# Kernel optimization log

Measured on AMD Instinct MI355X. Metric: run time of the kernel, lower is better.

The kernel has to match this reference:

```python
import jax, jax.numpy as jnp
import numpy as np
from functools import partial

DIM = 192
HEADS = 8
DN = ('NCHW', 'OIHW', 'NCHW')


def conv1x1(x, w):
    # w: [O, I, 1, 1]
    return jax.lax.conv_general_dilated(x, w, (1, 1), 'VALID', dimension_numbers=DN)


def dwconv3x3(x, w):
    # w: [C, 1, 3, 3], depthwise
    return jax.lax.conv_general_dilated(x, w, (1, 1), 'SAME', dimension_numbers=DN,
                                        feature_group_count=x.shape[1])


def l2norm(x, eps=1e-12):
    n = jnp.sqrt(jnp.sum(x * x, axis=-1, keepdims=True))
    return x / jnp.maximum(n, eps)


def compute_attention(q, k_s, v_s, k_c, v_c, temperature, beta):
    b, c, h, w = q.shape
    hw = h * w
    r = lambda t: t.reshape(b, HEADS, c // HEADS, hw)  # b head c (h w)
    qn = l2norm(r(q))
    ks = l2norm(r(k_s))
    kc = l2norm(r(k_c))
    vs, vc = r(v_s), r(v_c)
    # channel-wise attention: [b, head, c, c]
    sa = jax.nn.softmax(jnp.einsum('bhcn,bhdn->bhcd', qn, ks) * temperature, axis=-1)
    so = jnp.einsum('bhcd,bhdn->bhcn', sa, vs)
    ca = jax.nn.softmax(-(jnp.einsum('bhcn,bhdn->bhcd', qn, kc) * temperature), axis=-1)
    co = jnp.einsum('bhcd,bhdn->bhcn', ca, vc)
    out = jax.nn.sigmoid(beta) * so + co
    return out.reshape(b, c, h, w)


def setup_inputs() -> dict:
    key = jax.random.key(0)
    ks = jax.random.split(key, 8)
    B, C, H, W = 8, DIM, 128, 128
    s = 0.02
    return {
        'x1': jax.random.normal(ks[0], (B, C, H, W), jnp.float32),
        'x2': jax.random.normal(ks[1], (B, C, H, W), jnp.float32),
        'w_qkv1': jax.random.normal(ks[2], (3 * C, C, 1, 1), jnp.float32) * s,
        'w_dw1': jax.random.normal(ks[3], (3 * C, 1, 3, 3), jnp.float32) * s,
        'w_qkv2': jax.random.normal(ks[4], (3 * C, C, 1, 1), jnp.float32) * s,
        'w_dw2': jax.random.normal(ks[5], (3 * C, 1, 3, 3), jnp.float32) * s,
        'w_proj': jax.random.normal(ks[6], (C, C, 1, 1), jnp.float32) * s,
        'temperature': jnp.ones((HEADS, 1, 1), jnp.float32),
        'beta': jnp.zeros((1,), jnp.float32),
    }


def reference(x1, x2, w_qkv1, w_dw1, w_qkv2, w_dw2, w_proj, temperature, beta):
    qkv1 = dwconv3x3(conv1x1(x1, w_qkv1), w_dw1)
    q1, k1, v1 = jnp.split(qkv1, 3, axis=1)
    qkv2 = dwconv3x3(conv1x1(x2, w_qkv2), w_dw2)
    q2, k2, v2 = jnp.split(qkv2, 3, axis=1)
    e1 = compute_attention(q1, k1, v1, k2, v2, temperature, beta)
    e2 = compute_attention(q2, k2, v2, k1, v1, temperature, beta)
    return conv1x1(e1, w_proj), conv1x1(e2, w_proj)
```

## Files before the change

kernel.cpp:

```cpp
#include <hip/hip_runtime.h>

typedef unsigned short u16;
typedef unsigned int u32;

#define NB 8
#define NCH 192
#define NC3 576
#define NHW 16384
#define NHEADS 8

typedef __attribute__((ext_vector_type(8))) short s16x8;
typedef __attribute__((ext_vector_type(4))) float f32x4;

__device__ __forceinline__ float bf2f(u32 h) {
  return __uint_as_float(h << 16);
}
__device__ __forceinline__ u16 f2bf(float f) {
  u32 u = __float_as_uint(f);
  u = (u + 0x7fffu + ((u >> 16) & 1u)) >> 16;
  return (u16)u;
}
__device__ __forceinline__ u32 pk2(u16 a, u16 b) { return (u32)a | ((u32)b << 16); }

__device__ __forceinline__ int swz(int row) { return ((row >> 1) & 7) << 4; }

__device__ __forceinline__ void gl_lds16(const void* g, void* s) {
  __builtin_amdgcn_global_load_lds((const __attribute__((address_space(1))) unsigned int*)g,
                                   (__attribute__((address_space(3))) unsigned int*)s, 16, 0, 0);
}

__global__ __launch_bounds__(256) void wcast_kernel(
    const float* __restrict__ w1, const float* __restrict__ w2,
    u16* __restrict__ o1, u16* __restrict__ o2, float* __restrict__ norms2,
    float* __restrict__ G) {
  int i = blockIdx.x * 256 + threadIdx.x;
  if (i < NC3 * NCH) {
    o1[i] = f2bf(w1[i]);
    o2[i] = f2bf(w2[i]);
  }
  if (i < 4 * NB * NCH) norms2[i] = 0.f;
  if (i < NB * NHEADS * 2304) G[i] = 0.f;
}

__device__ __forceinline__ void conv_b_load(const float* __restrict__ x, int b, int nbase,
                                            int kb, int w, int l, float2 (&val)[16]) {
  const float* xr = x + (((size_t)(b * NCH + kb + w * 16)) << 14) + nbase + l * 2;
#pragma unroll
  for (int jj = 0; jj < 16; ++jj)
    val[jj] = *(const float2*)(xr + ((size_t)jj << 14));
}

__device__ __forceinline__ void conv_b_write(char* smem, int w, int l,
                                             const float2 (&val)[16]) {
#pragma unroll
  for (int nn = 0; nn < 2; ++nn) {
    const int row = l * 2 + nn;
    u32 p[8];
#pragma unroll
    for (int q = 0; q < 8; ++q) {
      const float a = nn ? val[2 * q].y : val[2 * q].x;
      const float bb = nn ? val[2 * q + 1].y : val[2 * q + 1].x;
      p[q] = pk2(f2bf(a), f2bf(bb));
    }
    char* base = smem + 24576 + row * 128;
    *(uint4*)(base + ((w * 32 + 0) ^ swz(row))) = make_uint4(p[0], p[1], p[2], p[3]);
    *(uint4*)(base + ((w * 32 + 16) ^ swz(row))) = make_uint4(p[4], p[5], p[6], p[7]);
  }
}

__device__ __forceinline__ void conv_a_glds(char* smem, const u16* __restrict__ wbf,
                                            int obase, int kb, int w, int l) {
#pragma unroll
  for (int i = 0; i < 6; ++i) {
    const int grp = i * 4 + w;
    const int row = grp * 8 + (l >> 3);
    const int cb = ((l & 7) * 16) ^ swz(row);
    const char* src = (const char*)wbf + (size_t)(obase + row) * 384 + kb * 2 + cb;
    gl_lds16(src, smem + grp * 1024);
  }
}

__global__ __launch_bounds__(256) void conv_mfma_kernel(
    const float* __restrict__ x1, const u16* __restrict__ wbf1, u16* __restrict__ pre1,
    const float* __restrict__ x2, const u16* __restrict__ wbf2, u16* __restrict__ pre2) {
  __shared__ char smem[40960];
  const int bid = blockIdx.x;
  const int id = (bid & 7) * 768 + (bid >> 3);
  const int mod = (id >= 3072) ? 1 : 0;
  const int idm = id - mod * 3072;
  const float* x = mod ? x2 : x1;
  const u16* wbf = mod ? wbf2 : wbf1;
  u16* pre = mod ? pre2 : pre1;
  const int b = idm / 384;
  const int rr = idm % 384;
  const int nbase = (rr / 3) * 128;
  const int obase = (rr % 3) * 192;
  const int tid = threadIdx.x;
  const int w = tid >> 6, l = tid & 63;
  const int wr = w >> 1, wc = w & 1;

  f32x4 acc[6][4];
#pragma unroll
  for (int m = 0; m < 6; ++m)
#pragma unroll
    for (int nf = 0; nf < 4; ++nf) acc[m][nf] = (f32x4)0.f;

  float2 fB[16];
  conv_b_load(x, b, nbase, 0, w, l, fB);

  for (int t = 0; t < 3; ++t) {
    conv_a_glds(smem, wbf, obase, t * 64, w, l);
    conv_b_write(smem, w, l, fB);
    if (t < 2) conv_b_load(x, b, nbase, (t + 1) * 64, w, l, fB);
    __syncthreads();
#pragma unroll
    for (int kk = 0; kk < 2; ++kk) {
      s16x8 a[6], bv[4];
      const int cbk = kk * 64 + (l >> 4) * 16;
#pragma unroll
      for (int m = 0; m < 6; ++m) {
        const int rowA = wr * 96 + m * 16 + (l & 15);
        a[m] = *(const s16x8*)(smem + rowA * 128 + (cbk ^ swz(rowA)));
      }
#pragma unroll
      for (int nf = 0; nf < 4; ++nf) {
        const int rowB = wc * 64 + nf * 16 + (l & 15);
        bv[nf] = *(const s16x8*)(smem + 24576 + rowB * 128 + (cbk ^ swz(rowB)));
      }
#pragma unroll
      for (int m = 0; m < 6; ++m)
#pragma unroll
        for (int nf = 0; nf < 4; ++nf)
          acc[m][nf] = __builtin_amdgcn_mfma_f32_16x16x32_bf16(a[m], bv[nf], acc[m][nf], 0, 0, 0);
    }
    __syncthreads();
  }
  u16* cw = (u16*)(smem) + w * 16 * 72;
#pragma unroll
  for (int m = 0; m < 6; ++m) {
#pragma unroll
    for (int nf = 0; nf < 4; ++nf)
#pragma unroll
      for (int r = 0; r < 4; ++r)
        cw[((l >> 4) * 4 + r) * 72 + nf * 16 + (l & 15)] = f2bf(acc[m][nf][r]);
#pragma unroll
    for (int p = 0; p < 2; ++p) {
      const int chunk = p * 64 + l;
      const int row = chunk >> 3, cg = chunk & 7;
      uint4 v = *(const uint4*)(cw + row * 72 + cg * 8);
      const int o = obase + wr * 96 + m * 16 + row;
      const int n = nbase + wc * 64 + cg * 8;
      *(uint4*)(pre + (((size_t)b * NC3 + o) << 14) + n) = v;
    }
  }
}

__device__ __forceinline__ void dw_body(float* red, const u16* __restrict__ in,
                                        const float* __restrict__ wdw, u16* __restrict__ out,
                                        float* __restrict__ norms2, const int mod,
                                        const size_t t, const int tid) {
  const int l = tid & 63;
  const int xc = (int)(t & 15);
  const int yp = (int)((t >> 4) & 63);
  const int bc = (int)(t >> 10);
  const int c = bc % NC3;
  const int b = bc / NC3;
  const u16* p = in + ((size_t)bc << 14);
  const float* wc = wdw + c * 9;
  const int x0 = xc * 8;
  const int y0 = yp * 2;

  float a[4][10];
#pragma unroll
  for (int r = 0; r < 4; ++r) {
    const int y2 = y0 + r - 1;
    if ((unsigned)y2 < 128u) {
      const u16* row = p + (y2 << 7);
      uint4 v = *(const uint4*)(row + x0);
      a[r][1] = bf2f(v.x & 0xffff); a[r][2] = bf2f(v.x >> 16);
      a[r][3] = bf2f(v.y & 0xffff); a[r][4] = bf2f(v.y >> 16);
      a[r][5] = bf2f(v.z & 0xffff); a[r][6] = bf2f(v.z >> 16);
      a[r][7] = bf2f(v.w & 0xffff); a[r][8] = bf2f(v.w >> 16);
    } else {
#pragma unroll
      for (int j = 1; j < 9; ++j) a[r][j] = 0.f;
    }
    const float lf = __shfl(a[r][8], (l - 1) & 63, 64);
    const float rt = __shfl(a[r][1], (l + 1) & 63, 64);
    a[r][0] = (xc > 0) ? lf : 0.f;
    a[r][9] = (xc < 15) ? rt : 0.f;
  }
  const float w00 = wc[0], w01 = wc[1], w02 = wc[2];
  const float w10 = wc[3], w11 = wc[4], w12 = wc[5];
  const float w20 = wc[6], w21 = wc[7], w22 = wc[8];
  float ssq = 0.f;
#pragma unroll
  for (int nn = 0; nn < 2; ++nn) {
    u16 o[8];
#pragma unroll
    for (int j = 0; j < 8; ++j) {
      float s = a[nn][j] * w00;
      s = fmaf(a[nn][j + 1], w01, s);
      s = fmaf(a[nn][j + 2], w02, s);
      s = fmaf(a[nn + 1][j], w10, s);
      s = fmaf(a[nn + 1][j + 1], w11, s);
      s = fmaf(a[nn + 1][j + 2], w12, s);
      s = fmaf(a[nn + 2][j], w20, s);
      s = fmaf(a[nn + 2][j + 1], w21, s);
      s = fmaf(a[nn + 2][j + 2], w22, s);
      ssq = fmaf(s, s, ssq);
      o[j] = f2bf(s);
    }
    *(uint4*)(out + ((size_t)bc << 14) + ((y0 + nn) << 7) + x0) =
        make_uint4(pk2(o[0], o[1]), pk2(o[2], o[3]), pk2(o[4], o[5]), pk2(o[6], o[7]));
  }

  if (c < 384) {
#pragma unroll
    for (int off = 32; off > 0; off >>= 1) ssq += __shfl_down(ssq, off, 64);
    if ((tid & 63) == 0) red[tid >> 6] = ssq;
    __syncthreads();
    if (tid == 0) {
      const int tt = (c < 192) ? mod : 2 + mod;
      atomicAdd(&norms2[(tt * NB + b) * NCH + (c % NCH)], red[0] + red[1] + red[2] + red[3]);
    }
  }
}

__global__ __launch_bounds__(256) void dwconv_kernel(
    const u16* __restrict__ in, const float* __restrict__ wdw, u16* __restrict__ out,
    float* __restrict__ norms2, const int mod) {
  __shared__ float red[4];
  dw_body(red, in, wdw, out, norms2, mod,
          (size_t)blockIdx.x * 256 + threadIdx.x, threadIdx.x);
}

__global__ __launch_bounds__(256) void dwm_kernel(
    const u16* __restrict__ pre1, const float* __restrict__ wdw1, u16* __restrict__ qkv1,
    const u16* __restrict__ pre2, const float* __restrict__ wdw2, u16* __restrict__ qkv2,
    float* __restrict__ norms2) {
  __shared__ float red[4];
  const size_t t = (size_t)blockIdx.x * 256 + threadIdx.x;
  const int bc = (int)(t >> 10);
  const int mod = (bc >= NB * NC3) ? 1 : 0;
  const size_t tm = t - ((size_t)mod * NB * NC3 << 10);
  if (mod)
    dw_body(red, pre2, wdw2, qkv2, norms2, 1, tm, threadIdx.x);
  else
    dw_body(red, pre1, wdw1, qkv1, norms2, 0, tm, threadIdx.x);
}

__global__ __launch_bounds__(256) void gram_mfma_kernel(
    const u16* __restrict__ qkv1, const u16* __restrict__ qkv2, float* __restrict__ G) {
  const int nc = blockIdx.x, h = blockIdx.y, b = blockIdx.z;
  const int tid = threadIdx.x;
  const int w = tid >> 6, l = tid & 63;

  const u16* qp[3];
  const u16* kp[3];
#pragma unroll
  for (int m = 0; m < 3; ++m) {
    const int rq = m * 16 + (l & 15);
    const int cc = h * 24 + (rq < 24 ? rq : rq - 24);
    const u16* basep = (rq < 24) ? qkv1 : qkv2;
    qp[m] = basep + (((size_t)b * NC3 + cc) << 14);
    kp[m] = basep + (((size_t)b * NC3 + 192 + cc) << 14);
  }
  const int kbase = nc * 1024 + w * 256 + (l >> 4) * 8;

  f32x4 acc[3][3];
#pragma unroll
  for (int m = 0; m < 3; ++m)
#pragma unroll
    for (int nf = 0; nf < 3; ++nf) acc[m][nf] = (f32x4)0.f;

  for (int t = 0; t < 8; ++t) {
    const int ko = kbase + t * 32;
    s16x8 a[3], bv[3];
#pragma unroll
    for (int m = 0; m < 3; ++m) {
      a[m] = *(const s16x8*)(qp[m] + ko);
      bv[m] = *(const s16x8*)(kp[m] + ko);
    }
#pragma unroll
    for (int m = 0; m < 3; ++m)
#pragma unroll
      for (int nf = 0; nf < 3; ++nf)
        acc[m][nf] = __builtin_amdgcn_mfma_f32_16x16x32_bf16(a[m], bv[nf], acc[m][nf], 0, 0, 0);
  }

  __shared__ float red[4][48][48];
#pragma unroll
  for (int m = 0; m < 3; ++m)
#pragma unroll
    for (int nf = 0; nf < 3; ++nf)
#pragma unroll
      for (int r = 0; r < 4; ++r)
        red[w][m * 16 + (l >> 4) * 4 + r][nf * 16 + (l & 15)] = acc[m][nf][r];
  __syncthreads();
  float* dst = G + ((size_t)b * 8 + h) * 2304;
  for (int e = tid; e < 2304; e += 256) {
    const int rr = e / 48, cc = e % 48;
    atomicAdd(&dst[e], red[0][rr][cc] + red[1][rr][cc] + red[2][rr][cc] + red[3][rr][cc]);
  }
}

__global__ __launch_bounds__(256) void softmax_wcat_kernel(
    const float* __restrict__ G, const float* __restrict__ norms2,
    const float* __restrict__ temperature, const float* __restrict__ beta,
    const float* __restrict__ wproj, u16* __restrict__ Wcat) {
  const int bh = blockIdx.x;
  const int b = bh >> 3, h = bh & 7;
  __shared__ float sm[4][24][24];
  __shared__ float nrm[4][24];
  const int tid = threadIdx.x;
  if (tid < 96) {
    int t = tid / 24, ci = tid % 24;
    nrm[t][ci] = fmaxf(sqrtf(norms2[(t * NB + b) * NCH + h * 24 + ci]), 1e-12f);
  }
  __syncthreads();
  const float T = temperature[h];
  const float sigB = 1.f / (1.f + expf(-beta[0]));
  if (tid < 96) {
    const int m = tid / 24, r = tid % 24;
    const float* Gb = G + (size_t)bh * 2304;
    const int gr = (m >= 2) ? 24 + r : r;
    const int gc0 = (m == 1 || m == 2) ? 24 : 0;
    const float* qn = (m >= 2) ? nrm[1] : nrm[0];
    const float* kn = (m == 1 || m == 2) ? nrm[3] : nrm[2];
    const float sign = (m == 0 || m == 2) ? 1.f : -1.f;
    const float qs = sign * T / qn[r];
    float L[24], mx = -1e30f;
#pragma unroll
    for (int cc = 0; cc < 24; ++cc) {
      L[cc] = Gb[gr * 48 + gc0 + cc] * qs / kn[cc];
      mx = fmaxf(mx, L[cc]);
    }
    float ssum = 0.f;
#pragma unroll
    for (int cc = 0; cc < 24; ++cc) {
      L[cc] = expf(L[cc] - mx);
      ssum += L[cc];
    }
    const float inv = 1.f / ssum;
#pragma unroll
    for (int cc = 0; cc < 24; ++cc) sm[m][r][cc] = L[cc] * inv;
  }
  __syncthreads();
  for (int e = tid; e < 384 * 48; e += 256) {
    const int o = e / 48, dc = e % 48;
    const int part = dc / 24, d = dc % 24;
    const int oc = (o < 192) ? o : o - 192;
    int m;
    float scale;
    if (o < 192) { m = part ? 1 : 0; scale = part ? 1.f : sigB; }
    else         { m = part ? 2 : 3; scale = part ? sigB : 1.f; }
    float s = 0.f;
#pragma unroll
    for (int ci = 0; ci < 24; ++ci) s += wproj[oc * 192 + h * 24 + ci] * sm[m][ci][d];
    Wcat[((size_t)b * 384 + o) * 384 + part * 192 + h * 24 + d] = f2bf(s * scale);
  }
}

__device__ __forceinline__ void fin_b_load(const u16* __restrict__ qkv1,
                                           const u16* __restrict__ qkv2,
                                           int b, int nbase, int kb, int w, int l,
                                           u32 (&val)[16]) {
  const u16* vbase = (kb < 192) ? qkv1 + (((size_t)b * NC3 + 384 + kb) << 14)
                                : qkv2 + (((size_t)b * NC3 + 384 + kb - 192) << 14);
  const u16* p0 = vbase + (((size_t)(w * 16)) << 14) + nbase + l * 2;
#pragma unroll
  for (int jj = 0; jj < 16; ++jj)
    val[jj] = *(const u32*)(p0 + ((size_t)jj << 14));
}

__device__ __forceinline__ void fin_b_write(char* smem, int w, int l,
                                            const u32 (&val)[16]) {
#pragma unroll
  for (int nn = 0; nn < 2; ++nn) {
    const int row = l * 2 + nn;
    u32 p[8];
#pragma unroll
    for (int q = 0; q < 8; ++q) {
      const u32 a = (val[2 * q] >> (nn * 16)) & 0xffffu;
      const u32 bb = (val[2 * q + 1] >> (nn * 16)) & 0xffffu;
      p[q] = a | (bb << 16);
    }
    char* base = smem + 32768 + row * 128;
    *(uint4*)(base + ((w * 32 + 0) ^ swz(row))) = make_uint4(p[0], p[1], p[2], p[3]);
    *(uint4*)(base + ((w * 32 + 16) ^ swz(row))) = make_uint4(p[4], p[5], p[6], p[7]);
  }
}

__device__ __forceinline__ void fin_a_glds(char* smem, const u16* __restrict__ Wcat,
                                           int b, int obase, int kb, int w, int l, int buf) {
#pragma unroll
  for (int i = 0; i < 4; ++i) {
    const int grp = i * 4 + w;
    const int row = grp * 8 + (l >> 3);
    const int cb = ((l & 7) * 16) ^ swz(row);
    const char* src = (const char*)Wcat + ((size_t)b * 384 + obase + row) * 768 + kb * 2 + cb;
    gl_lds16(src, smem + buf * 16384 + grp * 1024);
  }
}

__global__ __launch_bounds__(256) void final_mfma_kernel(
    const u16* __restrict__ qkv1, const u16* __restrict__ qkv2,
    const u16* __restrict__ Wcat, float* __restrict__ out) {
  __shared__ char smem[49152];
  const int bid = blockIdx.x;
  const int id = (bid & 7) * 384 + (bid >> 3);
  const int b = id / 384;
  const int rr2 = id % 384;
  const int nbase = (rr2 / 3) * 128;
  const int obase = (rr2 % 3) * 128;
  const int tid = threadIdx.x;
  const int w = tid >> 6, l = tid & 63;
  const int wr = w >> 1, wc = w & 1;

  f32x4 acc[4][4];
#pragma unroll
  for (int m = 0; m < 4; ++m)
#pragma unroll
    for (int nf = 0; nf < 4; ++nf) acc[m][nf] = (f32x4)0.f;

  u32 fV[16];
  fin_b_load(qkv1, qkv2, b, nbase, 0, w, l, fV);
  fin_a_glds(smem, Wcat, b, obase, 0, w, l, 0);
  fin_b_write(smem, w, l, fV);
  __syncthreads();

  for (int t = 0; t < 6; ++t) {
    const int cur = t & 1;
    const int nxt = cur ^ 1;
    if (t < 5) {
      fin_b_load(qkv1, qkv2, b, nbase, (t + 1) * 64, w, l, fV);
      fin_a_glds(smem, Wcat, b, obase, (t + 1) * 64, w, l, nxt);
    }
#pragma unroll
    for (int kk = 0; kk < 2; ++kk) {
      s16x8 a[4], bv[4];
      const int cbk = kk * 64 + (l >> 4) * 16;
#pragma unroll
      for (int m = 0; m < 4; ++m) {
        const int rowA = wr * 64 + m * 16 + (l & 15);
        a[m] = *(const s16x8*)(smem + cur * 16384 + rowA * 128 + (cbk ^ swz(rowA)));
      }
#pragma unroll
      for (int nf = 0; nf < 4; ++nf) {
        const int rowB = wc * 64 + nf * 16 + (l & 15);
        bv[nf] = *(const s16x8*)(smem + 32768 + rowB * 128 + (cbk ^ swz(rowB)));
      }
#pragma unroll
      for (int m = 0; m < 4; ++m)
#pragma unroll
        for (int nf = 0; nf < 4; ++nf)
          acc[m][nf] = __builtin_amdgcn_mfma_f32_16x16x32_bf16(a[m], bv[nf], acc[m][nf], 0, 0, 0);
    }
    __syncthreads();
    if (t < 5) {
      fin_b_write(smem, w, l, fV);
      __syncthreads();
    }
  }
  float* cw = (float*)(smem + w * 4352);
#pragma unroll
  for (int m = 0; m < 4; ++m) {
#pragma unroll
    for (int nf = 0; nf < 4; ++nf)
#pragma unroll
      for (int r = 0; r < 4; ++r)
        cw[((l >> 4) * 4 + r) * 68 + nf * 16 + (l & 15)] = acc[m][nf][r];
#pragma unroll
    for (int p = 0; p < 4; ++p) {
      const int chunk = p * 64 + l;
      const int row = chunk >> 4, cg = chunk & 15;
      f32x4 v = *(const f32x4*)(cw + row * 68 + cg * 4);
      const int o = obase + wr * 64 + m * 16 + row;
      const int n = nbase + wc * 64 + cg * 4;
      float* dst = (o < 192) ? out + (((size_t)b * NCH + o) << 14) + n
                             : out + 25165824 + (((size_t)b * NCH + o - 192) << 14) + n;
      __builtin_nontemporal_store(v, (f32x4*)dst);
    }
  }
}

extern "C" void kernel_launch(void* const* d_in, const int* in_sizes, int n_in,
                              void* d_out, int out_size, void* d_ws, size_t ws_size,
                              hipStream_t stream) {
  (void)in_sizes; (void)n_in; (void)out_size;
  const float* x1 = (const float*)d_in[0];
  const float* x2 = (const float*)d_in[1];
  const float* w_qkv1 = (const float*)d_in[2];
  const float* w_dw1 = (const float*)d_in[3];
  const float* w_qkv2 = (const float*)d_in[4];
  const float* w_dw2 = (const float*)d_in[5];
  const float* w_proj = (const float*)d_in[6];
  const float* temperature = (const float*)d_in[7];
  const float* beta = (const float*)d_in[8];
  float* out = (float*)d_out;

  char* wsb = (char*)d_ws;
  const size_t BUF = 150994944;
  const bool big = ws_size >= 607395840;

  u16* pre1 = (u16*)(wsb);
  u16* qkv1 = (u16*)(wsb + BUF);
  u16* pre2 = (u16*)(wsb + 2 * BUF);
  u16* qkv2 = big ? (u16*)(wsb + 3 * BUF) : pre1;
  char* tail = big ? (wsb + 4 * BUF) : (wsb + 3 * BUF);
  u16* wbf1 = (u16*)(tail);
  u16* wbf2 = (u16*)(tail + 221184);
  float* norms2 = (float*)(tail + 442368);
  float* G = (float*)(tail + 466944);
  u16* WcatBf = (u16*)(tail + 1056768);

  const int dwblocks = (int)(((size_t)NB * NC3 * NHW) / (256 * 16));

  wcast_kernel<<<576, 256, 0, stream>>>(w_qkv1, w_qkv2, wbf1, wbf2, norms2, G);
  conv_mfma_kernel<<<6144, 256, 0, stream>>>(x1, wbf1, pre1, x2, wbf2, pre2);
  if (big) {
    dwm_kernel<<<2 * dwblocks, 256, 0, stream>>>(pre1, w_dw1, qkv1, pre2, w_dw2, qkv2, norms2);
  } else {
    dwconv_kernel<<<dwblocks, 256, 0, stream>>>(pre1, w_dw1, qkv1, norms2, 0);
    dwconv_kernel<<<dwblocks, 256, 0, stream>>>(pre2, w_dw2, qkv2, norms2, 1);
  }
  gram_mfma_kernel<<<dim3(16, NHEADS, NB), 256, 0, stream>>>(qkv1, qkv2, G);
  softmax_wcat_kernel<<<NB * NHEADS, 256, 0, stream>>>(G, norms2, temperature, beta, w_proj, WcatBf);
  final_mfma_kernel<<<3072, 256, 0, stream>>>(qkv1, qkv2, WcatBf, out);
}
```

Measured before the change: 450.8 us.

## Keep full-K activation tile resident in LDS and loop over output tiles

```diff
diff --git a/kernel.cpp b/kernel.cpp
--- a/kernel.cpp
+++ b/kernel.cpp
@@ -42,116 +42,101 @@
   if (i < NB * NHEADS * 2304) G[i] = 0.f;
 }
 
-__device__ __forceinline__ void conv_b_load(const float* __restrict__ x, int b, int nbase,
-                                            int kb, int w, int l, float2 (&val)[16]) {
-  const float* xr = x + (((size_t)(b * NCH + kb + w * 16)) << 14) + nbase + l * 2;
-#pragma unroll
-  for (int jj = 0; jj < 16; ++jj)
-    val[jj] = *(const float2*)(xr + ((size_t)jj << 14));
-}
-
-__device__ __forceinline__ void conv_b_write(char* smem, int w, int l,
-                                             const float2 (&val)[16]) {
-#pragma unroll
-  for (int nn = 0; nn < 2; ++nn) {
-    const int row = l * 2 + nn;
-    u32 p[8];
-#pragma unroll
-    for (int q = 0; q < 8; ++q) {
-      const float a = nn ? val[2 * q].y : val[2 * q].x;
-      const float bb = nn ? val[2 * q + 1].y : val[2 * q + 1].x;
-      p[q] = pk2(f2bf(a), f2bf(bb));
-    }
-    char* base = smem + 24576 + row * 128;
-    *(uint4*)(base + ((w * 32 + 0) ^ swz(row))) = make_uint4(p[0], p[1], p[2], p[3]);
-    *(uint4*)(base + ((w * 32 + 16) ^ swz(row))) = make_uint4(p[4], p[5], p[6], p[7]);
-  }
-}
-
-__device__ __forceinline__ void conv_a_glds(char* smem, const u16* __restrict__ wbf,
-                                            int obase, int kb, int w, int l) {
-#pragma unroll
-  for (int i = 0; i < 6; ++i) {
-    const int grp = i * 4 + w;
-    const int row = grp * 8 + (l >> 3);
-    const int cb = ((l & 7) * 16) ^ swz(row);
-    const char* src = (const char*)wbf + (size_t)(obase + row) * 384 + kb * 2 + cb;
-    gl_lds16(src, smem + grp * 1024);
-  }
-}
-
 __global__ __launch_bounds__(256) void conv_mfma_kernel(
     const float* __restrict__ x1, const u16* __restrict__ wbf1, u16* __restrict__ pre1,
     const float* __restrict__ x2, const u16* __restrict__ wbf2, u16* __restrict__ pre2) {
-  __shared__ char smem[40960];
+  __shared__ char smem[49152];
   const int bid = blockIdx.x;
-  const int id = (bid & 7) * 768 + (bid >> 3);
-  const int mod = (id >= 3072) ? 1 : 0;
-  const int idm = id - mod * 3072;
+  const int id = (bid & 7) * 512 + (bid >> 3);
+  const int mod = (id >= 2048) ? 1 : 0;
+  const int idm = id - mod * 2048;
   const float* x = mod ? x2 : x1;
   const u16* wbf = mod ? wbf2 : wbf1;
   u16* pre = mod ? pre2 : pre1;
-  const int b = idm / 384;
-  const int rr = idm % 384;
-  const int nbase = (rr / 3) * 128;
-  const int obase = (rr % 3) * 192;
+  const int b = idm >> 8;
+  const int nbase = (idm & 255) * 64;
   const int tid = threadIdx.x;
   const int w = tid >> 6, l = tid & 63;
-  const int wr = w >> 1, wc = w & 1;
-
-  f32x4 acc[6][4];
-#pragma unroll
-  for (int m = 0; m < 6; ++m)
-#pragma unroll
-    for (int nf = 0; nf < 4; ++nf) acc[m][nf] = (f32x4)0.f;
-
-  float2 fB[16];
-  conv_b_load(x, b, nbase, 0, w, l, fB);
-
-  for (int t = 0; t < 3; ++t) {
-    conv_a_glds(smem, wbf, obase, t * 64, w, l);
-    conv_b_write(smem, w, l, fB);
-    if (t < 2) conv_b_load(x, b, nbase, (t + 1) * 64, w, l, fB);
+
+  {
+    const int row = l;
+    const int k0 = w * 48;
+    float v[48];
+#pragma unroll
+    for (int j = 0; j < 48; ++j)
+      v[j] = x[(((size_t)(b * NCH + k0 + j)) << 14) + nbase + row];
+    char* base = smem + row * 384;
+    const int sw = (row & 7) << 4;
+#pragma unroll
+    for (int q = 0; q < 6; ++q) {
+      uint4 pv = make_uint4(pk2(f2bf(v[q * 8 + 0]), f2bf(v[q * 8 + 1])),
+                            pk2(f2bf(v[q * 8 + 2]), f2bf(v[q * 8 + 3])),
+                            pk2(f2bf(v[q * 8 + 4]), f2bf(v[q * 8 + 5])),
+                            pk2(f2bf(v[q * 8 + 6]), f2bf(v[q * 8 + 7])));
+      *(uint4*)(base + ((w * 96 + q * 16) ^ sw)) = pv;
+    }
+  }
+
+  for (int ot = 0; ot < 3; ++ot) {
+    const int obase = ot * 192;
+    f32x4 acc[3][4];
+#pragma unroll
+    for (int m = 0; m < 3; ++m)
+#pragma unroll
+      for (int nf = 0; nf < 4; ++nf) acc[m][nf] = (f32x4)0.f;
+
+    for (int kt = 0; kt < 3; ++kt) {
+#pragma unroll
+      for (int i = 0; i < 6; ++i) {
+        const int grp = i * 4 + w;
+        const int row = grp * 8 + (l >> 3);
+        const int cb = ((l & 7) * 16) ^ swz(row);
+        const char* src = (const char*)wbf + (size_t)(obase + row) * 384 + kt * 128 + cb;
+        gl_lds16(src, smem + 24576 + grp * 1024);
+      }
+      __syncthreads();
+#pragma unroll
+      for (int kk = 0; kk < 2; ++kk) {
+        s16x8 a[3], bv[4];
+        const int cbkA = kk * 64 + (l >> 4) * 16;
+#pragma unroll
+        for (int m = 0; m < 3; ++m) {
+          const int rowA = w * 48 + m * 16 + (l & 15);
+          a[m] = *(const s16x8*)(smem + 24576 + rowA * 128 + (cbkA ^ swz(rowA)));
+        }
+        const int kOff = kt * 128 + kk * 64 + (l >> 4) * 16;
+#pragma unroll
+        for (int nf = 0; nf < 4; ++nf) {
+          const int rowB = nf * 16 + (l & 15);
+          bv[nf] = *(const s16x8*)(smem + rowB * 384 + (kOff ^ ((rowB & 7) << 4)));
+        }
+#pragma unroll
+        for (int m = 0; m < 3; ++m)
+#pragma unroll
+          for (int nf = 0; nf < 4; ++nf)
+            acc[m][nf] = __builtin_amdgcn_mfma_f32_16x16x32_bf16(a[m], bv[nf], acc[m][nf], 0, 0, 0);
+      }
+      __syncthreads();
+    }
+    u16* cw = (u16*)(smem + 24576) + w * 1152;
+#pragma unroll
+    for (int m = 0; m < 3; ++m) {
+#pragma unroll
+      for (int nf = 0; nf < 4; ++nf)
+#pragma unroll
+        for (int r = 0; r < 4; ++r)
+          cw[((l >> 4) * 4 + r) * 72 + nf * 16 + (l & 15)] = f2bf(acc[m][nf][r]);
+#pragma unroll
+      for (int p = 0; p < 2; ++p) {
+        const int chunk = p * 64 + l;
+        const int row = chunk >> 3, cg = chunk & 7;
+        uint4 vv = *(const uint4*)(cw + row * 72 + cg * 8);
+        const int o = obase + w * 48 + m * 16 + row;
+        const int n = nbase + cg * 8;
+        *(uint4*)(pre + (((size_t)b * NC3 + o) << 14) + n) = vv;
+      }
+    }
     __syncthreads();
-#pragma unroll
-    for (int kk = 0; kk < 2; ++kk) {
-      s16x8 a[6], bv[4];
-      const int cbk = kk * 64 + (l >> 4) * 16;
-#pragma unroll
-      for (int m = 0; m < 6; ++m) {
-        const int rowA = wr * 96 + m * 16 + (l & 15);
-        a[m] = *(const s16x8*)(smem + rowA * 128 + (cbk ^ swz(rowA)));
-      }
-#pragma unroll
-      for (int nf = 0; nf < 4; ++nf) {
-        const int rowB = wc * 64 + nf * 16 + (l & 15);
-        bv[nf] = *(const s16x8*)(smem + 24576 + rowB * 128 + (cbk ^ swz(rowB)));
-      }
-#pragma unroll
-      for (int m = 0; m < 6; ++m)
-#pragma unroll
-        for (int nf = 0; nf < 4; ++nf)
-          acc[m][nf] = __builtin_amdgcn_mfma_f32_16x16x32_bf16(a[m], bv[nf], acc[m][nf], 0, 0, 0);
-    }
-    __syncthreads();
-  }
-  u16* cw = (u16*)(smem) + w * 16 * 72;
-#pragma unroll
-  for (int m = 0; m < 6; ++m) {
-#pragma unroll
-    for (int nf = 0; nf < 4; ++nf)
-#pragma unroll
-      for (int r = 0; r < 4; ++r)
-        cw[((l >> 4) * 4 + r) * 72 + nf * 16 + (l & 15)] = f2bf(acc[m][nf][r]);
-#pragma unroll
-    for (int p = 0; p < 2; ++p) {
-      const int chunk = p * 64 + l;
-      const int row = chunk >> 3, cg = chunk & 7;
-      uint4 v = *(const uint4*)(cw + row * 72 + cg * 8);
-      const int o = obase + wr * 96 + m * 16 + row;
-      const int n = nbase + wc * 64 + cg * 8;
-      *(uint4*)(pre + (((size_t)b * NC3 + o) << 14) + n) = v;
-    }
   }
 }
 
@@ -518,7 +503,7 @@
   const int dwblocks = (int)(((size_t)NB * NC3 * NHW) / (256 * 16));
 
   wcast_kernel<<<576, 256, 0, stream>>>(w_qkv1, w_qkv2, wbf1, wbf2, norms2, G);
-  conv_mfma_kernel<<<6144, 256, 0, stream>>>(x1, wbf1, pre1, x2, wbf2, pre2);
+  conv_mfma_kernel<<<4096, 256, 0, stream>>>(x1, wbf1, pre1, x2, wbf2, pre2);
   if (big) {
     dwm_kernel<<<2 * dwblocks, 256, 0, stream>>>(pre1, w_dw1, qkv1, pre2, w_dw2, qkv2, norms2);
   } else {
```

Result: faster. 427.6 us (-5.1%).
